# Kernel optimization log

Hardware: AMD Instinct MI355X
Metric: run time of the kernel (lower is better)

## Reference

```python
import jax, jax.numpy as jnp
import numpy as np

B, S, C = 8192, 7, 30


def _iou(b1, b2):
    """Faithful replica of calculate_iou (including its intersect/area1 + area2 - intersect quirk).
    b1, b2: [..., 4] as (cx, cy, w, h). Returns [...] ."""
    area1 = b1[..., 2] * b1[..., 3]
    area2 = b2[..., 2] * b2[..., 3]
    max_left = jnp.maximum(b1[..., 0] - b1[..., 2] / 2, b2[..., 0] - b2[..., 2] / 2)
    min_right = jnp.minimum(b1[..., 0] + b1[..., 2] / 2, b2[..., 0] + b2[..., 2] / 2)
    max_top = jnp.maximum(b1[..., 1] - b1[..., 3] / 2, b2[..., 1] - b2[..., 3] / 2)
    min_bottom = jnp.minimum(b1[..., 1] + b1[..., 3] / 2, b2[..., 1] + b2[..., 3] / 2)
    inter = (min_right - max_left) * (min_bottom - max_top)
    overlap = (max_left < min_right) & (max_top < min_bottom)
    return jnp.where(overlap, inter / area1 + area2 - inter, 0.0)


def setup_inputs() -> dict:
    key = jax.random.key(0)
    k1, k2, k3 = jax.random.split(key, 3)
    preds = jax.random.uniform(k1, (B, S, S, C), dtype=jnp.float32, minval=0.01, maxval=1.0)
    labels = jax.random.uniform(k2, (B, S, S, C), dtype=jnp.float32, minval=0.01, maxval=1.0)
    obj = (jax.random.uniform(k3, (B, S, S)) < 0.3).astype(jnp.float32)
    labels = labels.at[..., 4].set(obj)  # objectness indicator in {0,1}
    return {"preds": preds, "labels": labels}


def reference(preds, labels):
    batch_size = labels.shape[0]
    obj = (labels[..., 4] == 1).astype(preds.dtype)  # [B,7,7]

    # IoUs are computed on detached values in the original (numpy round-trip)
    iou1 = jax.lax.stop_gradient(_iou(preds[..., 0:4], labels[..., 0:4]))
    iou2 = jax.lax.stop_gradient(_iou(preds[..., 5:9], labels[..., 5:9]))
    resp1 = iou1 > iou2  # box 1 responsible

    xy1 = jnp.sum((preds[..., 0:2] - labels[..., 0:2]) ** 2, axis=-1)
    xy2 = jnp.sum((preds[..., 5:7] - labels[..., 5:7]) ** 2, axis=-1)
    wh1 = jnp.sum((jnp.sqrt(preds[..., 2:4]) - jnp.sqrt(labels[..., 2:4])) ** 2, axis=-1)
    wh2 = jnp.sum((jnp.sqrt(preds[..., 7:9]) - jnp.sqrt(labels[..., 7:9])) ** 2, axis=-1)

    loss_xy = 5.0 * jnp.where(resp1, xy1, xy2)
    loss_wh = jnp.where(resp1, wh1, wh2)
    loss_obj = jnp.where(resp1, (preds[..., 4] - iou1) ** 2, (preds[..., 9] - iou2) ** 2)
    loss_noobj_objcell = 0.5 * jnp.where(resp1, (preds[..., 9] - iou2) ** 2, (preds[..., 4] - iou1) ** 2)
    loss_cls = jnp.sum((preds[..., 10:] - labels[..., 10:]) ** 2, axis=-1)

    obj_cell = loss_xy + loss_wh + loss_obj + loss_noobj_objcell + loss_cls
    noobj_cell = 0.5 * (preds[..., 4] ** 2 + preds[..., 9] ** 2)

    total = jnp.sum(obj * obj_cell + (1.0 - obj) * noobj_cell)
    return total / batch_size
```

## Files before the change

### kernel.cpp

```cpp
#include <hip/hip_runtime.h>

#define YB     8192
#define YS     7
#define YC     30
#define NCELLS (YB * YS * YS)
#define CPT    64
#define NBLK   (NCELLS / CPT)
#define BLOCK  256

__device__ __forceinline__ float iou_quirk(float cx1, float cy1, float w1, float h1,
                                           float cx2, float cy2, float w2, float h2) {
    float area1 = w1 * h1;
    float area2 = w2 * h2;
    float max_left   = fmaxf(cx1 - w1 * 0.5f, cx2 - w2 * 0.5f);
    float min_right  = fminf(cx1 + w1 * 0.5f, cx2 + w2 * 0.5f);
    float max_top    = fmaxf(cy1 - h1 * 0.5f, cy2 - h2 * 0.5f);
    float min_bottom = fminf(cy1 + h1 * 0.5f, cy2 + h2 * 0.5f);
    float inter = (min_right - max_left) * (min_bottom - max_top);
    bool overlap = (max_left < min_right) && (max_top < min_bottom);
    return overlap ? (inter / area1 + area2 - inter) : 0.0f;
}

__global__ __launch_bounds__(BLOCK) void yolo_partial_kernel(const float* __restrict__ preds,
                                                             const float* __restrict__ labels,
                                                             float* __restrict__ partial) {
    __shared__ float sp[CPT * YC];
    __shared__ float sl[CPT * YC];

    const int tid = threadIdx.x;
    const long base = (long)blockIdx.x * (CPT * YC);

    const float4* gp = (const float4*)(preds + base);
    const float4* gl = (const float4*)(labels + base);
    float4* sp4 = (float4*)sp;
    float4* sl4 = (float4*)sl;
    const int NV = CPT * YC / 4;

#if defined(__has_builtin) && __has_builtin(__builtin_amdgcn_global_load_lds)
    typedef const __attribute__((address_space(1))) void* as1_t;
    typedef __attribute__((address_space(3))) void* as3_t;
    for (int i = tid; i < NV; i += BLOCK)
        __builtin_amdgcn_global_load_lds((as1_t)(gp + i), (as3_t)(sp4 + i), 16, 0, 0);
    for (int i = tid; i < NV; i += BLOCK)
        __builtin_amdgcn_global_load_lds((as1_t)(gl + i), (as3_t)(sl4 + i), 16, 0, 0);
#else
    for (int i = tid; i < NV; i += BLOCK) {
        sp4[i] = gp[i];
        sl4[i] = gl[i];
    }
#endif
    __syncthreads();

    if (tid < CPT) {
        const float2* p2 = (const float2*)(sp + tid * YC);
        const float2* l2 = (const float2*)(sl + tid * YC);
        float pv[10], lv[10];
        #pragma unroll
        for (int i = 0; i < 5; ++i) {
            float2 a = p2[i]; pv[2 * i] = a.x; pv[2 * i + 1] = a.y;
            float2 b = l2[i]; lv[2 * i] = b.x; lv[2 * i + 1] = b.y;
        }
        float loss_cls = 0.0f;
        #pragma unroll
        for (int i = 5; i < 15; ++i) {
            float2 a = p2[i], b = l2[i];
            float dx = a.x - b.x, dy = a.y - b.y;
            loss_cls += dx * dx + dy * dy;
        }

        float iou1 = iou_quirk(pv[0], pv[1], pv[2], pv[3], lv[0], lv[1], lv[2], lv[3]);
        float iou2 = iou_quirk(pv[5], pv[6], pv[7], pv[8], lv[5], lv[6], lv[7], lv[8]);
        bool resp1 = iou1 > iou2;

        float dx1 = pv[0] - lv[0], dy1 = pv[1] - lv[1];
        float xy1 = dx1 * dx1 + dy1 * dy1;
        float dx2 = pv[5] - lv[5], dy2 = pv[6] - lv[6];
        float xy2 = dx2 * dx2 + dy2 * dy2;

        float sw1 = sqrtf(pv[2]) - sqrtf(lv[2]), sh1 = sqrtf(pv[3]) - sqrtf(lv[3]);
        float wh1 = sw1 * sw1 + sh1 * sh1;
        float sw2 = sqrtf(pv[7]) - sqrtf(lv[7]), sh2 = sqrtf(pv[8]) - sqrtf(lv[8]);
        float wh2 = sw2 * sw2 + sh2 * sh2;

        float d1 = pv[4] - iou1, d2 = pv[9] - iou2;
        float e1 = d1 * d1, e2 = d2 * d2;

        float loss_xy = 5.0f * (resp1 ? xy1 : xy2);
        float loss_wh = resp1 ? wh1 : wh2;
        float loss_obj = resp1 ? e1 : e2;
        float loss_noobj_objcell = 0.5f * (resp1 ? e2 : e1);

        float obj_cell = loss_xy + loss_wh + loss_obj + loss_noobj_objcell + loss_cls;
        float noobj_cell = 0.5f * (pv[4] * pv[4] + pv[9] * pv[9]);

        float v = (lv[4] == 1.0f) ? obj_cell : noobj_cell;

        for (int off = 32; off > 0; off >>= 1) v += __shfl_down(v, off);
        if (tid == 0) partial[blockIdx.x] = v;
    }
}

__global__ __launch_bounds__(BLOCK) void yolo_final_kernel(const float* __restrict__ partial,
                                                           float* __restrict__ out) {
    __shared__ double w[BLOCK / 64];
    double s = 0.0;
    for (int i = threadIdx.x; i < NBLK; i += BLOCK) s += (double)partial[i];
    for (int off = 32; off > 0; off >>= 1) s += __shfl_down(s, off);
    const int lane = threadIdx.x & 63, wid = threadIdx.x >> 6;
    if (lane == 0) w[wid] = s;
    __syncthreads();
    if (threadIdx.x == 0) out[0] = (float)((w[0] + w[1] + w[2] + w[3]) / (double)YB);
}

extern "C" void kernel_launch(void* const* d_in, const int* in_sizes, int n_in,
                              void* d_out, int out_size, void* d_ws, size_t ws_size,
                              hipStream_t stream) {
    const float* preds  = (const float*)d_in[0];
    const float* labels = (const float*)d_in[1];
    float* out = (float*)d_out;
    float* partial = (float*)d_ws;

    yolo_partial_kernel<<<NBLK, BLOCK, 0, stream>>>(preds, labels, partial);
    yolo_final_kernel<<<1, BLOCK, 0, stream>>>(partial, out);
}
```

Measured before the change: 27.90 us.

## Give each wavefront its own 64-cell LDS tile and drop the block barrier

Each of the four wavefronts in a block now loads its own 64-cell slice of preds and labels into a private LDS region and computes on it. Before, all 256 threads loaded one slice and only the first wave did the math. The block-wide __syncthreads is replaced by a per-wave s_waitcnt plus a sched_barrier, so waves proceed independently and all threads do useful compute. This quarters the block count and writes one partial per wave, at the cost of 4x LDS per block and reliance on the waitcnt being enough for async LDS loads to become visible.

New measurement: 28.91 us. +3.6%, slower.

```diff
diff --git a/kernel.cpp b/kernel.cpp
--- a/kernel.cpp
+++ b/kernel.cpp
@@ -4,9 +4,11 @@
 #define YS     7
 #define YC     30
 #define NCELLS (YB * YS * YS)
-#define CPT    64
-#define NBLK   (NCELLS / CPT)
+#define WCELLS 64
 #define BLOCK  256
+#define CPB    (4 * WCELLS)
+#define NBLK   (NCELLS / CPB)
+#define NPART  (NCELLS / WCELLS)
 
 __device__ __forceinline__ float iou_quirk(float cx1, float cy1, float w1, float h1,
                                            float cx2, float cy2, float w2, float h2) {
@@ -24,87 +26,90 @@
 __global__ __launch_bounds__(BLOCK) void yolo_partial_kernel(const float* __restrict__ preds,
                                                              const float* __restrict__ labels,
                                                              float* __restrict__ partial) {
-    __shared__ float sp[CPT * YC];
-    __shared__ float sl[CPT * YC];
+    __shared__ float lds[4][2][WCELLS * YC];
 
-    const int tid = threadIdx.x;
-    const long base = (long)blockIdx.x * (CPT * YC);
+    const int tid  = threadIdx.x;
+    const int lane = tid & 63;
+    const int w    = tid >> 6;
 
-    const float4* gp = (const float4*)(preds + base);
-    const float4* gl = (const float4*)(labels + base);
+    const long cell0 = (long)blockIdx.x * CPB + (long)w * WCELLS;
+    const float4* gp = (const float4*)(preds  + cell0 * YC);
+    const float4* gl = (const float4*)(labels + cell0 * YC);
+    float* sp = &lds[w][0][0];
+    float* sl = &lds[w][1][0];
     float4* sp4 = (float4*)sp;
     float4* sl4 = (float4*)sl;
-    const int NV = CPT * YC / 4;
+    const int NV = WCELLS * YC / 4;
 
 #if defined(__has_builtin) && __has_builtin(__builtin_amdgcn_global_load_lds)
     typedef const __attribute__((address_space(1))) void* as1_t;
     typedef __attribute__((address_space(3))) void* as3_t;
-    for (int i = tid; i < NV; i += BLOCK)
+    for (int i = lane; i < NV; i += 64)
         __builtin_amdgcn_global_load_lds((as1_t)(gp + i), (as3_t)(sp4 + i), 16, 0, 0);
-    for (int i = tid; i < NV; i += BLOCK)
+    for (int i = lane; i < NV; i += 64)
         __builtin_amdgcn_global_load_lds((as1_t)(gl + i), (as3_t)(sl4 + i), 16, 0, 0);
+    asm volatile("s_waitcnt vmcnt(0)" ::: "memory");
+    __builtin_amdgcn_sched_barrier(0);
 #else
-    for (int i = tid; i < NV; i += BLOCK) {
-        sp4[i] = gp[i];
-        sl4[i] = gl[i];
+    for (int i = lane; i < NV; i += 64) sp4[i] = gp[i];
+    for (int i = lane; i < NV; i += 64) sl4[i] = gl[i];
+    asm volatile("s_waitcnt vmcnt(0) lgkmcnt(0)" ::: "memory");
+    __builtin_amdgcn_sched_barrier(0);
+#endif
+
+    const float2* p2 = (const float2*)(sp + lane * YC);
+    const float2* l2 = (const float2*)(sl + lane * YC);
+
+    float pv[10], lv[10];
+    #pragma unroll
+    for (int i = 0; i < 5; ++i) {
+        float2 a = p2[i]; pv[2 * i] = a.x; pv[2 * i + 1] = a.y;
+        float2 b = l2[i]; lv[2 * i] = b.x; lv[2 * i + 1] = b.y;
     }
-#endif
-    __syncthreads();
+    float loss_cls = 0.0f;
+    #pragma unroll
+    for (int i = 5; i < 15; ++i) {
+        float2 a = p2[i], b = l2[i];
+        float dx = a.x - b.x, dy = a.y - b.y;
+        loss_cls += dx * dx + dy * dy;
+    }
 
-    if (tid < CPT) {
-        const float2* p2 = (const float2*)(sp + tid * YC);
-        const float2* l2 = (const float2*)(sl + tid * YC);
-        float pv[10], lv[10];
-        #pragma unroll
-        for (int i = 0; i < 5; ++i) {
-            float2 a = p2[i]; pv[2 * i] = a.x; pv[2 * i + 1] = a.y;
-            float2 b = l2[i]; lv[2 * i] = b.x; lv[2 * i + 1] = b.y;
-        }
-        float loss_cls = 0.0f;
-        #pragma unroll
-        for (int i = 5; i < 15; ++i) {
-            float2 a = p2[i], b = l2[i];
-            float dx = a.x - b.x, dy = a.y - b.y;
-            loss_cls += dx * dx + dy * dy;
-        }
+    float iou1 = iou_quirk(pv[0], pv[1], pv[2], pv[3], lv[0], lv[1], lv[2], lv[3]);
+    float iou2 = iou_quirk(pv[5], pv[6], pv[7], pv[8], lv[5], lv[6], lv[7], lv[8]);
+    bool resp1 = iou1 > iou2;
 
-        float iou1 = iou_quirk(pv[0], pv[1], pv[2], pv[3], lv[0], lv[1], lv[2], lv[3]);
-        float iou2 = iou_quirk(pv[5], pv[6], pv[7], pv[8], lv[5], lv[6], lv[7], lv[8]);
-        bool resp1 = iou1 > iou2;
+    float dx1 = pv[0] - lv[0], dy1 = pv[1] - lv[1];
+    float xy1 = dx1 * dx1 + dy1 * dy1;
+    float dx2 = pv[5] - lv[5], dy2 = pv[6] - lv[6];
+    float xy2 = dx2 * dx2 + dy2 * dy2;
 
-        float dx1 = pv[0] - lv[0], dy1 = pv[1] - lv[1];
-        float xy1 = dx1 * dx1 + dy1 * dy1;
-        float dx2 = pv[5] - lv[5], dy2 = pv[6] - lv[6];
-        float xy2 = dx2 * dx2 + dy2 * dy2;
+    float sw1 = sqrtf(pv[2]) - sqrtf(lv[2]), sh1 = sqrtf(pv[3]) - sqrtf(lv[3]);
+    float wh1 = sw1 * sw1 + sh1 * sh1;
+    float sw2 = sqrtf(pv[7]) - sqrtf(lv[7]), sh2 = sqrtf(pv[8]) - sqrtf(lv[8]);
+    float wh2 = sw2 * sw2 + sh2 * sh2;
 
-        float sw1 = sqrtf(pv[2]) - sqrtf(lv[2]), sh1 = sqrtf(pv[3]) - sqrtf(lv[3]);
-        float wh1 = sw1 * sw1 + sh1 * sh1;
-        float sw2 = sqrtf(pv[7]) - sqrtf(lv[7]), sh2 = sqrtf(pv[8]) - sqrtf(lv[8]);
-        float wh2 = sw2 * sw2 + sh2 * sh2;
+    float d1 = pv[4] - iou1, d2 = pv[9] - iou2;
+    float e1 = d1 * d1, e2 = d2 * d2;
 
-        float d1 = pv[4] - iou1, d2 = pv[9] - iou2;
-        float e1 = d1 * d1, e2 = d2 * d2;
+    float loss_xy = 5.0f * (resp1 ? xy1 : xy2);
+    float loss_wh = resp1 ? wh1 : wh2;
+    float loss_obj = resp1 ? e1 : e2;
+    float loss_noobj_objcell = 0.5f * (resp1 ? e2 : e1);
 
-        float loss_xy = 5.0f * (resp1 ? xy1 : xy2);
-        float loss_wh = resp1 ? wh1 : wh2;
-        float loss_obj = resp1 ? e1 : e2;
-        float loss_noobj_objcell = 0.5f * (resp1 ? e2 : e1);
+    float obj_cell = loss_xy + loss_wh + loss_obj + loss_noobj_objcell + loss_cls;
+    float noobj_cell = 0.5f * (pv[4] * pv[4] + pv[9] * pv[9]);
 
-        float obj_cell = loss_xy + loss_wh + loss_obj + loss_noobj_objcell + loss_cls;
-        float noobj_cell = 0.5f * (pv[4] * pv[4] + pv[9] * pv[9]);
+    float v = (lv[4] == 1.0f) ? obj_cell : noobj_cell;
 
-        float v = (lv[4] == 1.0f) ? obj_cell : noobj_cell;
-
-        for (int off = 32; off > 0; off >>= 1) v += __shfl_down(v, off);
-        if (tid == 0) partial[blockIdx.x] = v;
-    }
+    for (int off = 32; off > 0; off >>= 1) v += __shfl_down(v, off);
+    if (lane == 0) partial[blockIdx.x * 4 + w] = v;
 }
 
 __global__ __launch_bounds__(BLOCK) void yolo_final_kernel(const float* __restrict__ partial,
                                                            float* __restrict__ out) {
     __shared__ double w[BLOCK / 64];
     double s = 0.0;
-    for (int i = threadIdx.x; i < NBLK; i += BLOCK) s += (double)partial[i];
+    for (int i = threadIdx.x; i < NPART; i += BLOCK) s += (double)partial[i];
     for (int off = 32; off > 0; off >>= 1) s += __shfl_down(s, off);
     const int lane = threadIdx.x & 63, wid = threadIdx.x >> 6;
     if (lane == 0) w[wid] = s;
```
